# Performance work log

Measured on AMD Instinct MI355X. Metric: run time of the kernel, lower is better.

Reference implementation:

```python
import jax, jax.numpy as jnp
import numpy as np

HEADS = 16
HEAD_DIM = 64  # embed_size 1024 // 16


def setup_inputs() -> dict:
    key = jax.random.key(0)
    ks = jax.random.split(key, 6)
    N, S, E = 2, 2048, 1024
    return {
        "values": jax.random.normal(ks[0], (N, S, E), dtype=jnp.float32),
        "keys": jax.random.normal(ks[1], (N, S, E), dtype=jnp.float32),
        "queries": jax.random.normal(ks[2], (N, S, E), dtype=jnp.float32),
        "Wv": jax.random.normal(ks[3], (E, E), dtype=jnp.float32) * (E ** -0.5),
        "Wk": jax.random.normal(ks[4], (E, E), dtype=jnp.float32) * (E ** -0.5),
        "Wq": jax.random.normal(ks[5], (E, E), dtype=jnp.float32) * (E ** -0.5),
    }


def reference(values, keys, queries, Wv, Wk, Wq):
    N, Sq, E = queries.shape
    Sk = keys.shape[1]
    H, D = HEADS, HEAD_DIM
    # linear projections (torch Linear: x @ W^T), then split heads
    v = (values @ Wv.T).reshape(N, Sk, H, D)
    k = (keys @ Wk.T).reshape(N, Sk, H, D)
    q = (queries @ Wq.T).reshape(N, Sq, H, D)
    # QK^T -> [N, H, Q, K]
    scores = jnp.einsum("nqhd,nkhd->nhqk", q, k)
    # no mask (original forward takes mask=None path); scale by sqrt(head_dim)
    attn = jax.nn.softmax(scores / jnp.asarray(D, scores.dtype) ** 0.5, axis=-1)
    # AV -> [N, Q, H, D] -> [N, Q, E]; note: fc_out is never applied in the original forward
    out = jnp.einsum("nhql,nlhd->nqhd", attn, v).reshape(N, Sq, H * D)
    return out
```

## Files before the change

### kernel.cpp

```cpp
#include <hip/hip_runtime.h>
#include <math.h>

#define SEQ 2048
#define EMB 1024
#define NH  16
#define HD  64

typedef __attribute__((ext_vector_type(8))) short short8;
typedef __attribute__((ext_vector_type(4))) float f32x4;

static const size_t XE = (size_t)2 * SEQ * EMB;
static const size_t WE = (size_t)EMB * EMB;

static __device__ __forceinline__ short f2bf(float f) {
    unsigned u = __builtin_bit_cast(unsigned, f);
    u = u + 0x7fffu + ((u >> 16) & 1u);
    return (short)(u >> 16);
}

#if __has_builtin(__builtin_amdgcn_cvt_pk_bf16_f32)
typedef __attribute__((ext_vector_type(2))) __bf16 bf16x2;
static __device__ __forceinline__ unsigned pk2(float a, float b) {
    bf16x2 v = __builtin_amdgcn_cvt_pk_bf16_f32(a, b);
    return __builtin_bit_cast(unsigned, v);
}
#else
static __device__ __forceinline__ unsigned pk2(float a, float b) {
    return (unsigned)(unsigned short)f2bf(a) |
           ((unsigned)(unsigned short)f2bf(b) << 16);
}
#endif

static __device__ __forceinline__ short8 cvt8(float4 a, float4 b) {
    union { unsigned u[4]; short8 s; } r;
    r.u[0] = pk2(a.x, a.y); r.u[1] = pk2(a.z, a.w);
    r.u[2] = pk2(b.x, b.y); r.u[3] = pk2(b.z, b.w);
    return r.s;
}

static __device__ __forceinline__ void gload16(const void* g, void* l) {
    __builtin_amdgcn_global_load_lds(
        (const __attribute__((address_space(1))) void*)g,
        (__attribute__((address_space(3))) void*)l, 16, 0, 0);
}

__global__ __launch_bounds__(256)
void cvt_w(const float* __restrict__ s0, const float* __restrict__ s1,
           const float* __restrict__ s2, short* __restrict__ d) {
    int id = blockIdx.x;
    int seg = id >> 9, off = id & 511;
    const float* s = (seg == 0) ? s0 : (seg == 1) ? s1 : s2;
    short* dd = d + (size_t)seg * WE;
    size_t i = (size_t)off * 256 + threadIdx.x;
    const float4* sp = (const float4*)s;
    float4 a = sp[2 * i], b = sp[2 * i + 1];
    *(short8*)(dd + i * 8) = cvt8(a, b);
}

__global__ __launch_bounds__(256, 3)
void proj(const float* __restrict__ Xq, const float* __restrict__ Xk,
          const float* __restrict__ Xv, const short* __restrict__ Wb,
          short* __restrict__ qb, short* __restrict__ kbuf,
          short* __restrict__ vt) {
    __shared__ float4 Fs[2][1024];
    __shared__ short8 Hs[2][512];

    const int L = blockIdx.x;
    const int xcd = L & 7, i = L >> 3;
    const int z = i >> 5;
    const int m = i & 31;
    const int ty = xcd * 4 + (m & 3);
    const int tx = m >> 2;

    const float* Fop; const short* Hop; short* C;
    if (z == 0)      { Fop = Xq; Hop = Wb;           C = qb;   }
    else if (z == 1) { Fop = Xk; Hop = Wb + WE;      C = kbuf; }
    else             { Fop = Xv; Hop = Wb + 2 * WE;  C = vt;   }
    const int fr0 = ty * 128;
    const int hr0 = tx * 128;

    const int t = threadIdx.x, w = t >> 6, lane = t & 63;
    const int l15 = lane & 15, quad = lane >> 4;
    const int mh = (w >> 1) * 64, nh2 = (w & 1) * 64;

    auto stageF = [&](int p, int k0) {
#pragma unroll
        for (int j = 0; j < 4; ++j) {
            int g = j * 256 + t, row = g >> 3, c = g & 7;
            int cs = c ^ (row & 7);
            gload16(Fop + (size_t)(fr0 + row) * EMB + k0 + cs * 4,
                    &Fs[p][j * 256 + w * 64]);
        }
    };
    auto stageH = [&](int p, int k0) {
#pragma unroll
        for (int j = 0; j < 2; ++j) {
            int g = j * 256 + t, row = g & 127, c = g >> 7;
            gload16(Hop + (size_t)(hr0 + row) * EMB + k0 + c * 8,
                    &Hs[p][j * 256 + w * 64]);
        }
    };
    auto fragF = [&](int p, int fr) -> short8 {
        int r7 = fr & 7;
        float4 a = Fs[p][fr * 8 + ((2 * quad) ^ r7)];
        float4 b = Fs[p][fr * 8 + ((2 * quad + 1) ^ r7)];
        return cvt8(a, b);
    };

    f32x4 acc[4][4];
#pragma unroll
    for (int a = 0; a < 4; ++a)
#pragma unroll
        for (int b = 0; b < 4; ++b) acc[a][b] = 0.f;

    stageF(0, 0);
    stageH(0, 0);

    int p = 0;
    for (int k0 = 0; k0 < EMB; k0 += 32, p ^= 1) {
        __syncthreads();
        if (k0 + 32 < EMB) { stageF(p ^ 1, k0 + 32); stageH(p ^ 1, k0 + 32); }

        short8 af[4], bf[4];
        if (z < 2) {
#pragma unroll
            for (int mi = 0; mi < 4; ++mi)
                af[mi] = fragF(p, mh + mi * 16 + l15);
#pragma unroll
            for (int ni = 0; ni < 4; ++ni)
                bf[ni] = Hs[p][quad * 128 + nh2 + ni * 16 + l15];
        } else {
#pragma unroll
            for (int mi = 0; mi < 4; ++mi)
                af[mi] = Hs[p][quad * 128 + mh + mi * 16 + l15];
#pragma unroll
            for (int ni = 0; ni < 4; ++ni)
                bf[ni] = fragF(p, nh2 + ni * 16 + l15);
        }
#pragma unroll
        for (int mi = 0; mi < 4; ++mi)
#pragma unroll
            for (int ni = 0; ni < 4; ++ni)
                acc[mi][ni] = __builtin_amdgcn_mfma_f32_16x16x32_bf16(
                    af[mi], bf[ni], acc[mi][ni], 0, 0, 0);
    }

    const int am0 = (z < 2) ? fr0 : hr0;
    const int bn0 = (z < 2) ? hr0 : fr0;
#pragma unroll
    for (int mi = 0; mi < 4; ++mi)
#pragma unroll
        for (int ni = 0; ni < 4; ++ni)
#pragma unroll
            for (int r = 0; r < 4; ++r) {
                int gm = am0 + mh + mi * 16 + quad * 4 + r;
                int gn = bn0 + nh2 + ni * 16 + l15;
                short v = f2bf(acc[mi][ni][r]);
                if (z < 2) {
                    C[(size_t)gm * EMB + gn] = v;
                } else {
                    C[((size_t)(gn >> 11) * EMB + gm) * SEQ + (gn & 2047)] = v;
                }
            }
}

__global__ __launch_bounds__(256, 3)
void attn_mfma(const short* __restrict__ Qg, const short* __restrict__ Kg,
               const short* __restrict__ Vtg, float* __restrict__ OutD) {
    __shared__ short8 QPs[1024];
    __shared__ short8 Ks[2][512];
    __shared__ short8 Vs[2][512];

    const int t = threadIdx.x, w = t >> 6, lane = t & 63;
    const int l15 = lane & 15, quad = lane >> 4;
    const int L = blockIdx.x;
    const int xcd = L & 7, i = L >> 3;
    const int bh = xcd * 4 + (i & 3);
    const int q0 = (i >> 2) * 128;
    const int b = bh >> 4, h = bh & 15;
    const short* Qb = Qg + (size_t)b * SEQ * EMB + h * HD;
    const short* Kb = Kg + (size_t)b * SEQ * EMB + h * HD;
    const short* Vb = Vtg + ((size_t)b * EMB + h * HD) * SEQ;

#pragma unroll
    for (int j2 = 0; j2 < 4; ++j2) {
        int g = w * 4 + j2, c = g >> 1, row = (g & 1) * 64 + lane;
        gload16(Qb + (size_t)(q0 + row) * EMB + c * 8, &QPs[g * 64]);
    }
#pragma unroll
    for (int j2 = 0; j2 < 2; ++j2) {
        int c = w * 2 + j2;
        gload16(Kb + (size_t)lane * EMB + c * 8, &Ks[0][c * 64]);
        gload16(Vb + (size_t)lane * SEQ + c * 8, &Vs[0][c * 64]);
    }
    __syncthreads();

    short8 qf[2][2];
#pragma unroll
    for (int qi = 0; qi < 2; ++qi)
#pragma unroll
        for (int kb2 = 0; kb2 < 2; ++kb2)
            qf[qi][kb2] = QPs[(kb2 * 4 + quad) * 128 + w * 32 + qi * 16 + l15];
    __syncthreads();

    f32x4 o[2][4];
    float lr[2] = {0.f, 0.f};
#pragma unroll
    for (int qi = 0; qi < 2; ++qi)
#pragma unroll
        for (int ni = 0; ni < 4; ++ni) o[qi][ni] = 0.f;
    const float cl2 = 0.18033688011112042f;
    const float c0  = 11.541560327111707f;

    int p = 0;
    for (int kt = 0; kt < SEQ; kt += 64, p ^= 1) {
        if (kt) __syncthreads();
        if (kt + 64 < SEQ) {
#pragma unroll
            for (int j2 = 0; j2 < 2; ++j2) {
                int c = w * 2 + j2;
                gload16(Kb + (size_t)(kt + 64 + lane) * EMB + c * 8,
                        &Ks[p ^ 1][c * 64]);
                gload16(Vb + (size_t)lane * SEQ + kt + 64 + c * 8,
                        &Vs[p ^ 1][c * 64]);
            }
        }

        f32x4 s[4][2];
#pragma unroll
        for (int kblk = 0; kblk < 4; ++kblk)
#pragma unroll
            for (int qi = 0; qi < 2; ++qi) s[kblk][qi] = 0.f;
#pragma unroll
        for (int kb2 = 0; kb2 < 2; ++kb2) {
            short8 ak[4];
#pragma unroll
            for (int kblk = 0; kblk < 4; ++kblk)
                ak[kblk] = Ks[p][(kb2 * 4 + quad) * 64 + kblk * 16 + l15];
#pragma unroll
            for (int kblk = 0; kblk < 4; ++kblk)
#pragma unroll
                for (int qi = 0; qi < 2; ++qi)
                    s[kblk][qi] = __builtin_amdgcn_mfma_f32_16x16x32_bf16(
                        ak[kblk], qf[qi][kb2], s[kblk][qi], 0, 0, 0);
        }

#pragma unroll
        for (int qi = 0; qi < 2; ++qi) {
            int row = w * 32 + qi * 16 + l15;
#pragma unroll
            for (int kblk = 0; kblk < 4; ++kblk) {
                float p0 = __builtin_amdgcn_exp2f(fmaf(s[kblk][qi][0], cl2, -c0));
                float p1 = __builtin_amdgcn_exp2f(fmaf(s[kblk][qi][1], cl2, -c0));
                float p2 = __builtin_amdgcn_exp2f(fmaf(s[kblk][qi][2], cl2, -c0));
                float p3 = __builtin_amdgcn_exp2f(fmaf(s[kblk][qi][3], cl2, -c0));
                lr[qi] += (p0 + p1) + (p2 + p3);
                uint2 pv; pv.x = pk2(p0, p1); pv.y = pk2(p2, p3);
                int chunk = kblk * 2 + (quad >> 1);
                *(uint2*)((char*)QPs +
                          (((chunk * 128 + row) << 4) | ((quad & 1) << 3))) = pv;
            }
        }

#pragma unroll
        for (int kb2 = 0; kb2 < 2; ++kb2) {
            short8 ap[2], bv[4];
#pragma unroll
            for (int qi = 0; qi < 2; ++qi)
                ap[qi] = QPs[(kb2 * 4 + quad) * 128 + w * 32 + qi * 16 + l15];
#pragma unroll
            for (int ni = 0; ni < 4; ++ni)
                bv[ni] = Vs[p][(kb2 * 4 + quad) * 64 + ni * 16 + l15];
#pragma unroll
            for (int qi = 0; qi < 2; ++qi)
#pragma unroll
                for (int ni = 0; ni < 4; ++ni)
                    o[qi][ni] = __builtin_amdgcn_mfma_f32_16x16x32_bf16(
                        ap[qi], bv[ni], o[qi][ni], 0, 0, 0);
        }
    }

#pragma unroll
    for (int qi = 0; qi < 2; ++qi) {
        float l = lr[qi];
        l += __shfl_xor(l, 16);
        l += __shfl_xor(l, 32);
        lr[qi] = l;
    }
#pragma unroll
    for (int qi = 0; qi < 2; ++qi)
#pragma unroll
        for (int r = 0; r < 4; ++r) {
            float inv = 1.0f / __shfl(lr[qi], quad * 4 + r);
            int q = q0 + w * 32 + qi * 16 + quad * 4 + r;
            float* op = OutD + ((size_t)b * SEQ + q) * EMB + h * HD;
#pragma unroll
            for (int ni = 0; ni < 4; ++ni)
                op[ni * 16 + l15] = o[qi][ni][r] * inv;
        }
}

extern "C" void kernel_launch(void* const* d_in, const int* in_sizes, int n_in,
                              void* d_out, int out_size, void* d_ws, size_t ws_size,
                              hipStream_t stream) {
    const float* values  = (const float*)d_in[0];
    const float* keys    = (const float*)d_in[1];
    const float* queries = (const float*)d_in[2];
    const float* Wv      = (const float*)d_in[3];
    const float* Wk      = (const float*)d_in[4];
    const float* Wq      = (const float*)d_in[5];
    float* out = (float*)d_out;

    short* qb = (short*)d_ws;
    short* kb = qb + XE;
    short* vt = kb + XE;
    short* wb = vt + XE;

    cvt_w<<<1536, 256, 0, stream>>>(Wq, Wk, Wv, wb);
    proj<<<768, 256, 0, stream>>>(queries, keys, values, wb, qb, kb, vt);
    attn_mfma<<<512, 256, 0, stream>>>(qb, kb, vt, out);
}
```

Before: 212.8 us.

## Stage projection epilogue through LDS and halve attention query tile

Measured after the change: 231.3 us. 1.09x slower.

```diff
diff --git a/kernel.cpp b/kernel.cpp
--- a/kernel.cpp
+++ b/kernel.cpp
@@ -57,13 +57,16 @@
     *(short8*)(dd + i * 8) = cvt8(a, b);
 }
 
+#define ES_STRIDE 136
 __global__ __launch_bounds__(256, 3)
 void proj(const float* __restrict__ Xq, const float* __restrict__ Xk,
           const float* __restrict__ Xv, const short* __restrict__ Wb,
           short* __restrict__ qb, short* __restrict__ kbuf,
           short* __restrict__ vt) {
-    __shared__ float4 Fs[2][1024];
-    __shared__ short8 Hs[2][512];
+    __shared__ __align__(16) char lds_raw[49152];
+    float4* Fs = (float4*)lds_raw;
+    short8* Hs = (short8*)(lds_raw + 32768);
+    short*  Es = (short*)lds_raw;
 
     const int L = blockIdx.x;
     const int xcd = L & 7, i = L >> 3;
@@ -89,7 +92,7 @@
             int g = j * 256 + t, row = g >> 3, c = g & 7;
             int cs = c ^ (row & 7);
             gload16(Fop + (size_t)(fr0 + row) * EMB + k0 + cs * 4,
-                    &Fs[p][j * 256 + w * 64]);
+                    &Fs[p * 1024 + j * 256 + w * 64]);
         }
     };
     auto stageH = [&](int p, int k0) {
@@ -97,13 +100,13 @@
         for (int j = 0; j < 2; ++j) {
             int g = j * 256 + t, row = g & 127, c = g >> 7;
             gload16(Hop + (size_t)(hr0 + row) * EMB + k0 + c * 8,
-                    &Hs[p][j * 256 + w * 64]);
+                    &Hs[p * 512 + j * 256 + w * 64]);
         }
     };
     auto fragF = [&](int p, int fr) -> short8 {
         int r7 = fr & 7;
-        float4 a = Fs[p][fr * 8 + ((2 * quad) ^ r7)];
-        float4 b = Fs[p][fr * 8 + ((2 * quad + 1) ^ r7)];
+        float4 a = Fs[p * 1024 + fr * 8 + ((2 * quad) ^ r7)];
+        float4 b = Fs[p * 1024 + fr * 8 + ((2 * quad + 1) ^ r7)];
         return cvt8(a, b);
     };
 
@@ -128,11 +131,11 @@
                 af[mi] = fragF(p, mh + mi * 16 + l15);
 #pragma unroll
             for (int ni = 0; ni < 4; ++ni)
-                bf[ni] = Hs[p][quad * 128 + nh2 + ni * 16 + l15];
+                bf[ni] = Hs[p * 512 + quad * 128 + nh2 + ni * 16 + l15];
         } else {
 #pragma unroll
             for (int mi = 0; mi < 4; ++mi)
-                af[mi] = Hs[p][quad * 128 + mh + mi * 16 + l15];
+                af[mi] = Hs[p * 512 + quad * 128 + mh + mi * 16 + l15];
 #pragma unroll
             for (int ni = 0; ni < 4; ++ni)
                 bf[ni] = fragF(p, nh2 + ni * 16 + l15);
@@ -145,29 +148,38 @@
                     af[mi], bf[ni], acc[mi][ni], 0, 0, 0);
     }
 
-    const int am0 = (z < 2) ? fr0 : hr0;
-    const int bn0 = (z < 2) ? hr0 : fr0;
+    __syncthreads();
 #pragma unroll
     for (int mi = 0; mi < 4; ++mi)
 #pragma unroll
         for (int ni = 0; ni < 4; ++ni)
 #pragma unroll
             for (int r = 0; r < 4; ++r) {
-                int gm = am0 + mh + mi * 16 + quad * 4 + r;
-                int gn = bn0 + nh2 + ni * 16 + l15;
-                short v = f2bf(acc[mi][ni][r]);
-                if (z < 2) {
-                    C[(size_t)gm * EMB + gn] = v;
-                } else {
-                    C[((size_t)(gn >> 11) * EMB + gm) * SEQ + (gn & 2047)] = v;
-                }
+                int lr_ = mh + mi * 16 + quad * 4 + r;
+                int lc_ = nh2 + ni * 16 + l15;
+                Es[lr_ * ES_STRIDE + lc_] = f2bf(acc[mi][ni][r]);
             }
-}
-
-__global__ __launch_bounds__(256, 3)
+    __syncthreads();
+    {
+        int row = t >> 1, half = t & 1;
+        const short* src = Es + row * ES_STRIDE + half * 64;
+        short* dst;
+        if (z < 2) {
+            dst = C + (size_t)(fr0 + row) * EMB + hr0 + half * 64;
+        } else {
+            int bz = fr0 >> 11, s0 = fr0 & 2047;
+            dst = C + ((size_t)bz * EMB + hr0 + row) * SEQ + s0 + half * 64;
+        }
+#pragma unroll
+        for (int j = 0; j < 8; ++j)
+            *(short8*)(dst + j * 8) = *(const short8*)(src + j * 8);
+    }
+}
+
+__global__ __launch_bounds__(256, 4)
 void attn_mfma(const short* __restrict__ Qg, const short* __restrict__ Kg,
                const short* __restrict__ Vtg, float* __restrict__ OutD) {
-    __shared__ short8 QPs[1024];
+    __shared__ short8 QPs[512];
     __shared__ short8 Ks[2][512];
     __shared__ short8 Vs[2][512];
 
@@ -176,39 +188,30 @@
     const int L = blockIdx.x;
     const int xcd = L & 7, i = L >> 3;
     const int bh = xcd * 4 + (i & 3);
-    const int q0 = (i >> 2) * 128;
+    const int q0 = (i >> 2) * 64;
     const int b = bh >> 4, h = bh & 15;
     const short* Qb = Qg + (size_t)b * SEQ * EMB + h * HD;
     const short* Kb = Kg + (size_t)b * SEQ * EMB + h * HD;
     const short* Vb = Vtg + ((size_t)b * EMB + h * HD) * SEQ;
 
 #pragma unroll
-    for (int j2 = 0; j2 < 4; ++j2) {
-        int g = w * 4 + j2, c = g >> 1, row = (g & 1) * 64 + lane;
-        gload16(Qb + (size_t)(q0 + row) * EMB + c * 8, &QPs[g * 64]);
-    }
-#pragma unroll
     for (int j2 = 0; j2 < 2; ++j2) {
         int c = w * 2 + j2;
+        gload16(Qb + (size_t)(q0 + lane) * EMB + c * 8, &QPs[c * 64]);
         gload16(Kb + (size_t)lane * EMB + c * 8, &Ks[0][c * 64]);
         gload16(Vb + (size_t)lane * SEQ + c * 8, &Vs[0][c * 64]);
     }
     __syncthreads();
 
-    short8 qf[2][2];
-#pragma unroll
-    for (int qi = 0; qi < 2; ++qi)
-#pragma unroll
-        for (int kb2 = 0; kb2 < 2; ++kb2)
-            qf[qi][kb2] = QPs[(kb2 * 4 + quad) * 128 + w * 32 + qi * 16 + l15];
-    __syncthreads();
-
-    f32x4 o[2][4];
-    float lr[2] = {0.f, 0.f};
-#pragma unroll
-    for (int qi = 0; qi < 2; ++qi)
-#pragma unroll
-        for (int ni = 0; ni < 4; ++ni) o[qi][ni] = 0.f;
+    short8 qf[2];
+#pragma unroll
+    for (int kb2 = 0; kb2 < 2; ++kb2)
+        qf[kb2] = QPs[(kb2 * 4 + quad) * 64 + w * 16 + l15];
+
+    f32x4 o[4];
+    float lr = 0.f;
+#pragma unroll
+    for (int ni = 0; ni < 4; ++ni) o[ni] = 0.f;
     const float cl2 = 0.18033688011112042f;
     const float c0  = 11.541560327111707f;
 
@@ -226,11 +229,9 @@
             }
         }
 
-        f32x4 s[4][2];
-#pragma unroll
-        for (int kblk = 0; kblk < 4; ++kblk)
-#pragma unroll
-            for (int qi = 0; qi < 2; ++qi) s[kblk][qi] = 0.f;
+        f32x4 s[4];
+#pragma unroll
+        for (int kblk = 0; kblk < 4; ++kblk) s[kblk] = 0.f;
 #pragma unroll
         for (int kb2 = 0; kb2 < 2; ++kb2) {
             short8 ak[4];
@@ -239,65 +240,51 @@
                 ak[kblk] = Ks[p][(kb2 * 4 + quad) * 64 + kblk * 16 + l15];
 #pragma unroll
             for (int kblk = 0; kblk < 4; ++kblk)
-#pragma unroll
-                for (int qi = 0; qi < 2; ++qi)
-                    s[kblk][qi] = __builtin_amdgcn_mfma_f32_16x16x32_bf16(
-                        ak[kblk], qf[qi][kb2], s[kblk][qi], 0, 0, 0);
-        }
-
-#pragma unroll
-        for (int qi = 0; qi < 2; ++qi) {
-            int row = w * 32 + qi * 16 + l15;
+                s[kblk] = __builtin_amdgcn_mfma_f32_16x16x32_bf16(
+                    ak[kblk], qf[kb2], s[kblk], 0, 0, 0);
+        }
+
+        {
+            int row = w * 16 + l15;
 #pragma unroll
             for (int kblk = 0; kblk < 4; ++kblk) {
-                float p0 = __builtin_amdgcn_exp2f(fmaf(s[kblk][qi][0], cl2, -c0));
-                float p1 = __builtin_amdgcn_exp2f(fmaf(s[kblk][qi][1], cl2, -c0));
-                float p2 = __builtin_amdgcn_exp2f(fmaf(s[kblk][qi][2], cl2, -c0));
-                float p3 = __builtin_amdgcn_exp2f(fmaf(s[kblk][qi][3], cl2, -c0));
-                lr[qi] += (p0 + p1) + (p2 + p3);
+                float p0 = __builtin_amdgcn_exp2f(fmaf(s[kblk][0], cl2, -c0));
+                float p1 = __builtin_amdgcn_exp2f(fmaf(s[kblk][1], cl2, -c0));
+                float p2 = __builtin_amdgcn_exp2f(fmaf(s[kblk][2], cl2, -c0));
+                float p3 = __builtin_amdgcn_exp2f(fmaf(s[kblk][3], cl2, -c0));
+                lr += (p0 + p1) + (p2 + p3);
                 uint2 pv; pv.x = pk2(p0, p1); pv.y = pk2(p2, p3);
                 int chunk = kblk * 2 + (quad >> 1);
                 *(uint2*)((char*)QPs +
-                          (((chunk * 128 + row) << 4) | ((quad & 1) << 3))) = pv;
+                          (((chunk * 64 + row) << 4) | ((quad & 1) << 3))) = pv;
             }
         }
 
 #pragma unroll
         for (int kb2 = 0; kb2 < 2; ++kb2) {
-            short8 ap[2], bv[4];
-#pragma unroll
-            for (int qi = 0; qi < 2; ++qi)
-                ap[qi] = QPs[(kb2 * 4 + quad) * 128 + w * 32 + qi * 16 + l15];
+            short8 ap = QPs[(kb2 * 4 + quad) * 64 + w * 16 + l15];
+            short8 bv[4];
 #pragma unroll
             for (int ni = 0; ni < 4; ++ni)
                 bv[ni] = Vs[p][(kb2 * 4 + quad) * 64 + ni * 16 + l15];
 #pragma unroll
-            for (int qi = 0; qi < 2; ++qi)
-#pragma unroll
-                for (int ni = 0; ni < 4; ++ni)
-                    o[qi][ni] = __builtin_amdgcn_mfma_f32_16x16x32_bf16(
-                        ap[qi], bv[ni], o[qi][ni], 0, 0, 0);
-        }
-    }
-
-#pragma unroll
-    for (int qi = 0; qi < 2; ++qi) {
-        float l = lr[qi];
-        l += __shfl_xor(l, 16);
-        l += __shfl_xor(l, 32);
-        lr[qi] = l;
-    }
-#pragma unroll
-    for (int qi = 0; qi < 2; ++qi)
-#pragma unroll
-        for (int r = 0; r < 4; ++r) {
-            float inv = 1.0f / __shfl(lr[qi], quad * 4 + r);
-            int q = q0 + w * 32 + qi * 16 + quad * 4 + r;
-            float* op = OutD + ((size_t)b * SEQ + q) * EMB + h * HD;
-#pragma unroll
-            for (int ni = 0; ni < 4; ++ni)
-                op[ni * 16 + l15] = o[qi][ni][r] * inv;
-        }
+            for (int ni = 0; ni < 4; ++ni)
+                o[ni] = __builtin_amdgcn_mfma_f32_16x16x32_bf16(
+                    ap, bv[ni], o[ni], 0, 0, 0);
+        }
+    }
+
+    lr += __shfl_xor(lr, 16);
+    lr += __shfl_xor(lr, 32);
+#pragma unroll
+    for (int r = 0; r < 4; ++r) {
+        float inv = 1.0f / __shfl(lr, quad * 4 + r);
+        int q = q0 + w * 16 + quad * 4 + r;
+        float* op = OutD + ((size_t)b * SEQ + q) * EMB + h * HD;
+#pragma unroll
+        for (int ni = 0; ni < 4; ++ni)
+            op[ni * 16 + l15] = o[ni][r] * inv;
+    }
 }
 
 extern "C" void kernel_launch(void* const* d_in, const int* in_sizes, int n_in,
@@ -318,5 +305,5 @@
 
     cvt_w<<<1536, 256, 0, stream>>>(Wq, Wk, Wv, wb);
     proj<<<768, 256, 0, stream>>>(queries, keys, values, wb, qb, kb, vt);
-    attn_mfma<<<512, 256, 0, stream>>>(qb, kb, vt, out);
-}
+    attn_mfma<<<1024, 256, 0, stream>>>(qb, kb, vt, out);
+}
```

## Stage projection epilogue through LDS and widen attention K/V tiles with swizzle

Applied to the files above, without the earlier changes.

Result: no change. 208.8 us (-1.9%).

```diff
diff --git a/kernel.cpp b/kernel.cpp
--- a/kernel.cpp
+++ b/kernel.cpp
@@ -57,13 +57,16 @@
     *(short8*)(dd + i * 8) = cvt8(a, b);
 }
 
+#define ES_STRIDE 136
 __global__ __launch_bounds__(256, 3)
 void proj(const float* __restrict__ Xq, const float* __restrict__ Xk,
           const float* __restrict__ Xv, const short* __restrict__ Wb,
           short* __restrict__ qb, short* __restrict__ kbuf,
           short* __restrict__ vt) {
-    __shared__ float4 Fs[2][1024];
-    __shared__ short8 Hs[2][512];
+    __shared__ __align__(16) char lds_raw[49152];
+    float4* Fs = (float4*)lds_raw;
+    short8* Hs = (short8*)(lds_raw + 32768);
+    short*  Es = (short*)lds_raw;
 
     const int L = blockIdx.x;
     const int xcd = L & 7, i = L >> 3;
@@ -89,7 +92,7 @@
             int g = j * 256 + t, row = g >> 3, c = g & 7;
             int cs = c ^ (row & 7);
             gload16(Fop + (size_t)(fr0 + row) * EMB + k0 + cs * 4,
-                    &Fs[p][j * 256 + w * 64]);
+                    &Fs[p * 1024 + j * 256 + w * 64]);
         }
     };
     auto stageH = [&](int p, int k0) {
@@ -97,13 +100,13 @@
         for (int j = 0; j < 2; ++j) {
             int g = j * 256 + t, row = g & 127, c = g >> 7;
             gload16(Hop + (size_t)(hr0 + row) * EMB + k0 + c * 8,
-                    &Hs[p][j * 256 + w * 64]);
+                    &Hs[p * 512 + j * 256 + w * 64]);
         }
     };
     auto fragF = [&](int p, int fr) -> short8 {
         int r7 = fr & 7;
-        float4 a = Fs[p][fr * 8 + ((2 * quad) ^ r7)];
-        float4 b = Fs[p][fr * 8 + ((2 * quad + 1) ^ r7)];
+        float4 a = Fs[p * 1024 + fr * 8 + ((2 * quad) ^ r7)];
+        float4 b = Fs[p * 1024 + fr * 8 + ((2 * quad + 1) ^ r7)];
         return cvt8(a, b);
     };
 
@@ -128,11 +131,11 @@
                 af[mi] = fragF(p, mh + mi * 16 + l15);
 #pragma unroll
             for (int ni = 0; ni < 4; ++ni)
-                bf[ni] = Hs[p][quad * 128 + nh2 + ni * 16 + l15];
+                bf[ni] = Hs[p * 512 + quad * 128 + nh2 + ni * 16 + l15];
         } else {
 #pragma unroll
             for (int mi = 0; mi < 4; ++mi)
-                af[mi] = Hs[p][quad * 128 + mh + mi * 16 + l15];
+                af[mi] = Hs[p * 512 + quad * 128 + mh + mi * 16 + l15];
 #pragma unroll
             for (int ni = 0; ni < 4; ++ni)
                 bf[ni] = fragF(p, nh2 + ni * 16 + l15);
@@ -145,34 +148,44 @@
                     af[mi], bf[ni], acc[mi][ni], 0, 0, 0);
     }
 
-    const int am0 = (z < 2) ? fr0 : hr0;
-    const int bn0 = (z < 2) ? hr0 : fr0;
+    __syncthreads();
 #pragma unroll
     for (int mi = 0; mi < 4; ++mi)
 #pragma unroll
         for (int ni = 0; ni < 4; ++ni)
 #pragma unroll
             for (int r = 0; r < 4; ++r) {
-                int gm = am0 + mh + mi * 16 + quad * 4 + r;
-                int gn = bn0 + nh2 + ni * 16 + l15;
-                short v = f2bf(acc[mi][ni][r]);
-                if (z < 2) {
-                    C[(size_t)gm * EMB + gn] = v;
-                } else {
-                    C[((size_t)(gn >> 11) * EMB + gm) * SEQ + (gn & 2047)] = v;
-                }
+                int lr_ = mh + mi * 16 + quad * 4 + r;
+                int lc_ = nh2 + ni * 16 + l15;
+                Es[lr_ * ES_STRIDE + lc_] = f2bf(acc[mi][ni][r]);
             }
-}
-
-__global__ __launch_bounds__(256, 3)
+    __syncthreads();
+    {
+        int row = t >> 1, half = t & 1;
+        const short* src = Es + row * ES_STRIDE + half * 64;
+        short* dst;
+        if (z < 2) {
+            dst = C + (size_t)(fr0 + row) * EMB + hr0 + half * 64;
+        } else {
+            int bz = fr0 >> 11, s0 = fr0 & 2047;
+            dst = C + ((size_t)bz * EMB + hr0 + row) * SEQ + s0 + half * 64;
+        }
+#pragma unroll
+        for (int j = 0; j < 8; ++j)
+            *(short8*)(dst + j * 8) = *(const short8*)(src + j * 8);
+    }
+}
+
+__global__ __launch_bounds__(256, 2)
 void attn_mfma(const short* __restrict__ Qg, const short* __restrict__ Kg,
                const short* __restrict__ Vtg, float* __restrict__ OutD) {
     __shared__ short8 QPs[1024];
-    __shared__ short8 Ks[2][512];
-    __shared__ short8 Vs[2][512];
+    __shared__ short8 Ks[2][1024];
+    __shared__ short8 Vs[2][1024];
 
     const int t = threadIdx.x, w = t >> 6, lane = t & 63;
     const int l15 = lane & 15, quad = lane >> 4;
+    const int lr3 = lane >> 3, lc7 = lane & 7;
     const int L = blockIdx.x;
     const int xcd = L & 7, i = L >> 3;
     const int bh = xcd * 4 + (i & 3);
@@ -182,26 +195,38 @@
     const short* Kb = Kg + (size_t)b * SEQ * EMB + h * HD;
     const short* Vb = Vtg + ((size_t)b * EMB + h * HD) * SEQ;
 
-#pragma unroll
-    for (int j2 = 0; j2 < 4; ++j2) {
-        int g = w * 4 + j2, c = g >> 1, row = (g & 1) * 64 + lane;
-        gload16(Qb + (size_t)(q0 + row) * EMB + c * 8, &QPs[g * 64]);
-    }
-#pragma unroll
-    for (int j2 = 0; j2 < 2; ++j2) {
-        int c = w * 2 + j2;
-        gload16(Kb + (size_t)lane * EMB + c * 8, &Ks[0][c * 64]);
-        gload16(Vb + (size_t)lane * SEQ + c * 8, &Vs[0][c * 64]);
-    }
+    auto stageKV = [&](int p, int kt) {
+#pragma unroll
+        for (int j = 0; j < 4; ++j) {
+            int rb = w * 32 + j * 8;
+            int krow = rb + lr3;
+            gload16(Kb + (size_t)(kt + krow) * EMB + ((lc7 ^ (krow & 7)) * 8),
+                    &Ks[p][rb * 8]);
+            int half = w >> 1, db = (w & 1) * 32 + j * 8;
+            int d = db + lr3;
+            gload16(Vb + (size_t)d * SEQ + kt + half * 64 + ((lc7 ^ (d & 7)) * 8),
+                    &Vs[p][half * 512 + db * 8]);
+        }
+    };
+
+#pragma unroll
+    for (int j = 0; j < 4; ++j) {
+        int rb = w * 32 + j * 8;
+        int row = rb + lr3;
+        gload16(Qb + (size_t)(q0 + row) * EMB + ((lc7 ^ (row & 7)) * 8),
+                &QPs[rb * 8]);
+    }
+    stageKV(0, 0);
     __syncthreads();
 
     short8 qf[2][2];
 #pragma unroll
     for (int qi = 0; qi < 2; ++qi)
 #pragma unroll
-        for (int kb2 = 0; kb2 < 2; ++kb2)
-            qf[qi][kb2] = QPs[(kb2 * 4 + quad) * 128 + w * 32 + qi * 16 + l15];
-    __syncthreads();
+        for (int kb2 = 0; kb2 < 2; ++kb2) {
+            int row = w * 32 + qi * 16 + l15;
+            qf[qi][kb2] = QPs[row * 8 + ((kb2 * 4 + quad) ^ (l15 & 7))];
+        }
 
     f32x4 o[2][4];
     float lr[2] = {0.f, 0.f};
@@ -213,70 +238,72 @@
     const float c0  = 11.541560327111707f;
 
     int p = 0;
-    for (int kt = 0; kt < SEQ; kt += 64, p ^= 1) {
+    for (int kt = 0; kt < SEQ; kt += 128, p ^= 1) {
         if (kt) __syncthreads();
-        if (kt + 64 < SEQ) {
-#pragma unroll
-            for (int j2 = 0; j2 < 2; ++j2) {
-                int c = w * 2 + j2;
-                gload16(Kb + (size_t)(kt + 64 + lane) * EMB + c * 8,
-                        &Ks[p ^ 1][c * 64]);
-                gload16(Vb + (size_t)lane * SEQ + kt + 64 + c * 8,
-                        &Vs[p ^ 1][c * 64]);
+        if (kt + 128 < SEQ) stageKV(p ^ 1, kt + 128);
+
+#pragma unroll
+        for (int half = 0; half < 2; ++half) {
+            f32x4 s[4][2];
+#pragma unroll
+            for (int kblk = 0; kblk < 4; ++kblk)
+#pragma unroll
+                for (int qi = 0; qi < 2; ++qi) s[kblk][qi] = 0.f;
+#pragma unroll
+            for (int kb2 = 0; kb2 < 2; ++kb2) {
+                short8 ak[4];
+#pragma unroll
+                for (int kblk = 0; kblk < 4; ++kblk) {
+                    int row = half * 64 + kblk * 16 + l15;
+                    ak[kblk] = Ks[p][row * 8 + ((kb2 * 4 + quad) ^ (l15 & 7))];
+                }
+#pragma unroll
+                for (int kblk = 0; kblk < 4; ++kblk)
+#pragma unroll
+                    for (int qi = 0; qi < 2; ++qi)
+                        s[kblk][qi] = __builtin_amdgcn_mfma_f32_16x16x32_bf16(
+                            ak[kblk], qf[qi][kb2], s[kblk][qi], 0, 0, 0);
             }
-        }
-
-        f32x4 s[4][2];
-#pragma unroll
-        for (int kblk = 0; kblk < 4; ++kblk)
-#pragma unroll
-            for (int qi = 0; qi < 2; ++qi) s[kblk][qi] = 0.f;
-#pragma unroll
-        for (int kb2 = 0; kb2 < 2; ++kb2) {
-            short8 ak[4];
-#pragma unroll
-            for (int kblk = 0; kblk < 4; ++kblk)
-                ak[kblk] = Ks[p][(kb2 * 4 + quad) * 64 + kblk * 16 + l15];
-#pragma unroll
-            for (int kblk = 0; kblk < 4; ++kblk)
+
+#pragma unroll
+            for (int qi = 0; qi < 2; ++qi) {
+                int row = w * 32 + qi * 16 + l15;
+#pragma unroll
+                for (int kblk = 0; kblk < 4; ++kblk) {
+                    float p0 = __builtin_amdgcn_exp2f(fmaf(s[kblk][qi][0], cl2, -c0));
+                    float p1 = __builtin_amdgcn_exp2f(fmaf(s[kblk][qi][1], cl2, -c0));
+                    float p2 = __builtin_amdgcn_exp2f(fmaf(s[kblk][qi][2], cl2, -c0));
+                    float p3 = __builtin_amdgcn_exp2f(fmaf(s[kblk][qi][3], cl2, -c0));
+                    lr[qi] += (p0 + p1) + (p2 + p3);
+                    uint2 pv; pv.x = pk2(p0, p1); pv.y = pk2(p2, p3);
+                    int kc = kblk * 2 + (quad >> 1);
+                    *(uint2*)((char*)QPs +
+                        (((row * 8 + (kc ^ (l15 & 7))) << 4) | ((quad & 1) << 3)))
+                        = pv;
+                }
+            }
+
+#pragma unroll
+            for (int kb2 = 0; kb2 < 2; ++kb2) {
+                short8 ap[2], bv[4];
+#pragma unroll
+                for (int qi = 0; qi < 2; ++qi) {
+                    int row = w * 32 + qi * 16 + l15;
+                    ap[qi] = QPs[row * 8 + ((kb2 * 4 + quad) ^ (l15 & 7))];
+                }
+#pragma unroll
+                for (int ni = 0; ni < 4; ++ni) {
+                    int dr = ni * 16 + l15;
+                    bv[ni] = Vs[p][half * 512 + dr * 8 +
+                                   ((kb2 * 4 + quad) ^ (l15 & 7))];
+                }
 #pragma unroll
                 for (int qi = 0; qi < 2; ++qi)
-                    s[kblk][qi] = __builtin_amdgcn_mfma_f32_16x16x32_bf16(
-                        ak[kblk], qf[qi][kb2], s[kblk][qi], 0, 0, 0);
-        }
-
-#pragma unroll
-        for (int qi = 0; qi < 2; ++qi) {
-            int row = w * 32 + qi * 16 + l15;
-#pragma unroll
-            for (int kblk = 0; kblk < 4; ++kblk) {
-                float p0 = __builtin_amdgcn_exp2f(fmaf(s[kblk][qi][0], cl2, -c0));
-                float p1 = __builtin_amdgcn_exp2f(fmaf(s[kblk][qi][1], cl2, -c0));
-                float p2 = __builtin_amdgcn_exp2f(fmaf(s[kblk][qi][2], cl2, -c0));
-                float p3 = __builtin_amdgcn_exp2f(fmaf(s[kblk][qi][3], cl2, -c0));
-                lr[qi] += (p0 + p1) + (p2 + p3);
-                uint2 pv; pv.x = pk2(p0, p1); pv.y = pk2(p2, p3);
-                int chunk = kblk * 2 + (quad >> 1);
-                *(uint2*)((char*)QPs +
-                          (((chunk * 128 + row) << 4) | ((quad & 1) << 3))) = pv;
+#pragma unroll
+                    for (int ni = 0; ni < 4; ++ni)
+                        o[qi][ni] = __builtin_amdgcn_mfma_f32_16x16x32_bf16(
+                            ap[qi], bv[ni], o[qi][ni], 0, 0, 0);
             }
-        }
-
-#pragma unroll
-        for (int kb2 = 0; kb2 < 2; ++kb2) {
-            short8 ap[2], bv[4];
-#pragma unroll
-            for (int qi = 0; qi < 2; ++qi)
-                ap[qi] = QPs[(kb2 * 4 + quad) * 128 + w * 32 + qi * 16 + l15];
-#pragma unroll
-            for (int ni = 0; ni < 4; ++ni)
-                bv[ni] = Vs[p][(kb2 * 4 + quad) * 64 + ni * 16 + l15];
-#pragma unroll
-            for (int qi = 0; qi < 2; ++qi)
-#pragma unroll
-                for (int ni = 0; ni < 4; ++ni)
-                    o[qi][ni] = __builtin_amdgcn_mfma_f32_16x16x32_bf16(
-                        ap[qi], bv[ni], o[qi][ni], 0, 0, 0);
         }
     }
 
```
